# Kernel tuning notes

Hardware: AMD Instinct MI355X
Metric: run time of the kernel (lower is better)

The kernel has to match this reference:

```python
import jax, jax.numpy as jnp
import numpy as np

B, L, D = 2048, 64, 128
NODES = 512
EPS = 1e-6


def setup_inputs() -> dict:
    key = jax.random.key(0)
    ks = jax.random.split(key, 9)
    src_ids = jax.random.randint(ks[0], (B, L), 0, NODES, dtype=jnp.int32)
    dst_ids = jax.random.randint(ks[1], (B, L), 0, NODES, dtype=jnp.int32)
    src_node_ids = jax.random.randint(ks[2], (B,), 1, NODES, dtype=jnp.int32)
    dst_node_ids = jax.random.randint(ks[3], (B,), 1, NODES, dtype=jnp.int32)
    node_interact_times = 100.0 + jax.random.uniform(ks[4], (B,), jnp.float32)
    src_times = jax.random.uniform(ks[5], (B, L), jnp.float32) * 100.0
    dst_times = jax.random.uniform(ks[6], (B, L), jnp.float32) * 100.0
    W1 = jax.random.normal(ks[7], (1, D), jnp.float32) * 0.5
    b1 = jnp.zeros((D,), jnp.float32)
    W2 = jax.random.normal(ks[8], (D, D), jnp.float32) * (1.0 / np.sqrt(D))
    b2 = jnp.zeros((D,), jnp.float32)
    return dict(src_padded_nodes_neighbor_ids=src_ids,
                dst_padded_nodes_neighbor_ids=dst_ids,
                src_node_ids=src_node_ids, dst_node_ids=dst_node_ids,
                node_interact_times=node_interact_times,
                src_padded_nodes_neighbor_times=src_times,
                dst_padded_nodes_neighbor_times=dst_times,
                W1=W1, b1=b1, W2=W2, b2=b2)


def _group_stats(ids, t):
    # per-position stats of the group sharing the same neighbor id. ids,t: (L,)
    n_pos = ids.shape[0]
    eq = ids[:, None] == ids[None, :]                       # (L,L) group membership
    n = eq.sum(1)                                           # group size at each position
    nf = n.astype(t.dtype)
    tb = jnp.broadcast_to(t[None, :], (n_pos, n_pos))
    tmax = jnp.max(jnp.where(eq, tb, -jnp.inf), axis=1)
    tmin = jnp.min(jnp.where(eq, tb, jnp.inf), axis=1)
    # mean(diff(sorted(ts))) == (max-min)/(n-1)
    avg_iat = jnp.where(n > 1, (tmax - tmin) / jnp.maximum(nf - 1.0, 1.0), 0.0)
    # stable rank of each element inside its own group (order statistic)
    pos = jnp.arange(n_pos)
    before = (t[:, None] < t[None, :]) | ((t[:, None] == t[None, :]) & (pos[:, None] < pos[None, :]))
    rank = jnp.sum(eq & before, axis=0)
    split = n // 2
    sel = eq & (rank[None, :] == split[:, None])            # exactly one per group
    t_split = jnp.sum(jnp.where(sel, tb, 0.0), axis=1)      # sorted(ts)[n//2]
    denom = jnp.maximum(nf - split.astype(t.dtype) - 1.0, 1.0)
    recent_iat = jnp.where(n >= 4, (tmax - t_split) / denom, 0.0)
    valid = ids != 0                                        # dicts skip neighbor id 0
    return nf, jnp.where(valid, avg_iat, 0.0), jnp.where(valid, recent_iat, 0.0)


def _cross_lookup(ids_a, ids_b, vals_b):
    # dict.get(nid, 0.0) over the other side's per-group values (id 0 excluded)
    match = (ids_a[:, None] == ids_b[None, :]) & (ids_b[None, :] != 0)
    idx = jnp.argmax(match, axis=1)
    return jnp.where(match.any(1), vals_b[idx], 0.0)


def _last_time(ids_a, ids_b, t_b):
    # dict comprehension keeps the LAST occurrence's timestamp (id 0 excluded)
    match = (ids_a[:, None] == ids_b[None, :]) & (ids_b[None, :] != 0)
    score = jnp.where(match, jnp.arange(ids_b.shape[0])[None, :], -1)
    li = score.max(1)
    return jnp.where(li >= 0, t_b[jnp.maximum(li, 0)], 0.0)


def _side_features(ids_a, t_a, ids_b, t_b, other_node_id, cur_t,
                   n_a, avg_a, rec_a, avg_b, rec_b, other_first):
    ft = t_a.dtype
    c_self = n_a
    c_other = jnp.sum(ids_a[:, None] == ids_b[None, :], axis=1).astype(ft)
    is_other = (ids_a == other_node_id).astype(ft)
    connects = (c_other > 0).astype(ft)
    freq_asym = jnp.where(c_other > 0, c_self / (c_other + EPS), 0.0)
    rcy_self = cur_t - t_a
    rcy_other = cur_t - _last_time(ids_a, ids_b, t_b)
    temp_asym = jnp.where(rcy_self > EPS, rcy_other / (rcy_self + EPS), 0.0)
    iat_other = _cross_lookup(ids_a, ids_b, avg_b)
    iat_asym = jnp.where(iat_other > EPS, avg_a / (iat_other + EPS), 0.0)
    riat_other = _cross_lookup(ids_a, ids_b, rec_b)
    riat_asym = jnp.where(riat_other > EPS, rec_a / (riat_other + EPS), 0.0)
    if other_first:
        head = [c_other, c_self]
    else:
        head = [c_self, c_other]
    return jnp.stack(head + [is_other, connects, freq_asym, temp_asym, iat_asym, riat_asym], axis=1)


def _per_sample(ids_s, ids_d, sid, did, cur_t, t_s, t_d):
    n_s, avg_s, rec_s = _group_stats(ids_s, t_s)
    n_d, avg_d, rec_d = _group_stats(ids_d, t_d)
    f_src = _side_features(ids_s, t_s, ids_d, t_d, did, cur_t,
                           n_s, avg_s, rec_s, avg_d, rec_d, False)
    f_dst = _side_features(ids_d, t_d, ids_s, t_s, sid, cur_t,
                           n_d, avg_d, rec_d, avg_s, rec_s, True)
    return f_src, f_dst


def _mlp_sum(feats, W1, b1, W2, b2):
    # Linear(1->D) -> ReLU -> Linear(D->D), applied per scalar feature, summed over the 8 features
    h = jax.nn.relu(feats[..., None] * W1[0] + b1)           # [B,L,8,D]
    y = jnp.einsum('blfd,de->blfe', h, W2) + b2
    return y.sum(axis=2)                                      # [B,L,D]


def reference(src_padded_nodes_neighbor_ids, dst_padded_nodes_neighbor_ids,
              src_node_ids, dst_node_ids, node_interact_times,
              src_padded_nodes_neighbor_times, dst_padded_nodes_neighbor_times,
              W1, b1, W2, b2):
    f_src, f_dst = jax.vmap(_per_sample)(
        src_padded_nodes_neighbor_ids, dst_padded_nodes_neighbor_ids,
        src_node_ids, dst_node_ids, node_interact_times,
        src_padded_nodes_neighbor_times, dst_padded_nodes_neighbor_times)
    f_src = jnp.where((src_padded_nodes_neighbor_ids == 0)[..., None], 0.0, f_src)
    f_dst = jnp.where((dst_padded_nodes_neighbor_ids == 0)[..., None], 0.0, f_dst)
    src_path_features = _mlp_sum(f_src, W1, b1, W2, b2)
    dst_path_features = _mlp_sum(f_dst, W1, b1, W2, b2)
    return src_path_features, dst_path_features
```

## Files before the change

kernel.cpp:

```cpp
#include <hip/hip_runtime.h>


#define EPSF 1e-6f
#define LDB 136

typedef __attribute__((ext_vector_type(8))) short bf16x8;
typedef __attribute__((ext_vector_type(4))) float f32x4;
typedef __attribute__((ext_vector_type(2))) float f32x2;

__device__ inline short f2bf(float x) {
    unsigned u = __float_as_uint(x);
    return (short)((u + 0x7fffu + ((u >> 16) & 1u)) >> 16);
}

__global__ void w2t_prep(const float* __restrict__ W2, short* __restrict__ w2t) {
    const int idx = blockIdx.x * 256 + threadIdx.x;
    const int k = idx >> 7, n = idx & 127;
    w2t[n * 128 + k] = f2bf(W2[idx]);
}

__launch_bounds__(128)
__global__ void lpe_feats(const int* __restrict__ src_ids,
                          const int* __restrict__ dst_ids,
                          const int* __restrict__ src_nid,
                          const int* __restrict__ dst_nid,
                          const float* __restrict__ t_now,
                          const float* __restrict__ src_t,
                          const float* __restrict__ dst_t,
                          float* __restrict__ fs)
{
    __shared__ int2  s_idt[128];
    __shared__ __align__(16) f32x4 s_tab[2][512];

    const int tid  = threadIdx.x;
    const int b    = blockIdx.x;
    const int side = tid >> 6;
    const int i    = tid & 63;

    #pragma unroll
    for (int u = tid; u < 1024; u += 128) ((float*)s_tab)[u * 4] = 0.f;

    const float cur = t_now[b];
    const int   s_n = src_nid[b], d_n = dst_nid[b];

    const int*   idp = side ? dst_ids : src_ids;
    const float* tp  = side ? dst_t   : src_t;
    const int   my_id = idp[b * 64 + i];
    const float my_t  = tp [b * 64 + i];
    s_idt[tid] = make_int2(my_id, __float_as_int(my_t));
    __syncthreads();

    int n = 0, rank = 0, later = 0;
    float tmax = -3.4e38f, tmin = 3.4e38f;
    const int sbase = side * 64;
    #pragma unroll 8
    for (int j = 0; j < 64; ++j) {
        const int2 e = s_idt[sbase + j];
        const float tj = __int_as_float(e.y);
        if (e.x == my_id) {
            ++n;
            tmax = fmaxf(tmax, tj);
            tmin = fminf(tmin, tj);
            if (tj < my_t || (tj == my_t && j < i)) ++rank;
            if (j > i) later = 1;
        }
    }
    const float nf    = (float)n;
    const int   split = n >> 1;
    const float avg   = (n > 1) ? (tmax - tmin) / (nf - 1.f) : 0.f;
    if (my_id != 0) {
        s_tab[side][my_id].x = nf;
        s_tab[side][my_id].y = avg;
        if (rank == split)
            s_tab[side][my_id].z = (n >= 4)
                ? (tmax - my_t) / fmaxf(nf - (float)split - 1.f, 1.f) : 0.f;
        if (!later)
            s_tab[side][my_id].w = my_t;
    }
    __syncthreads();

    const int os = side ^ 1;
    const float rec_m = (my_id != 0) ? s_tab[side][my_id].z : 0.f;
    const f32x4 to = s_tab[os][my_id];
    const float n_o = (my_id != 0) ? to.x : 0.f;
    const bool  hit = n_o > 0.f;
    const float avg_o = hit ? to.y : 0.f;
    const float rec_o = hit ? to.z : 0.f;
    const float lastt = hit ? to.w : 0.f;
    const int other_node = side ? s_n : d_n;
    const float m = (my_id != 0) ? 1.f : 0.f;

    const float rcy_s = cur - my_t;
    const float rcy_o = cur - lastt;
    f32x4 f0, f1;
    f0.x = m * nf;
    f0.y = m * n_o;
    f0.z = m * ((my_id == other_node) ? 1.f : 0.f);
    f0.w = m * (hit ? 1.f : 0.f);
    f1.x = m * (hit ? nf / (n_o + EPSF) : 0.f);
    f1.y = m * ((rcy_s > EPSF) ? rcy_o / (rcy_s + EPSF) : 0.f);
    f1.z = m * ((avg_o > EPSF) ? avg / (avg_o + EPSF) : 0.f);
    f1.w = m * ((rec_o > EPSF) ? rec_m / (rec_o + EPSF) : 0.f);

    const long rowf = (long)side * 131072 + (long)b * 64 + i;
    *(f32x4*)&fs[rowf * 8]     = f0;
    *(f32x4*)&fs[rowf * 8 + 4] = f1;
}

__launch_bounds__(256, 3)
__global__ void lpe_gemm(const float* __restrict__ fs,
                         const short* __restrict__ w2t,
                         const float* __restrict__ W1,
                         const float* __restrict__ b1,
                         const float* __restrict__ b2,
                         float* __restrict__ out)
{
    __shared__ __align__(16) float s_w1[128], s_b1[128], s_b2[128];
    __shared__ __align__(16) short W2T[128 * LDB];
    __shared__ __align__(16) float s_stage[4][32][32];

    const int tid  = threadIdx.x;
    const int lane = tid & 63, wv = tid >> 6;
    const int quad = lane >> 4, ln = lane & 15;

    #pragma unroll
    for (int it = 0; it < 8; ++it) {
        const int c = tid + it * 256;
        const int n = c >> 4, j = c & 15;
        *(bf16x8*)&W2T[n * LDB + j * 8] = *(const bf16x8*)&w2t[n * 128 + j * 8];
    }
    if (tid < 128) { s_w1[tid] = W1[tid]; s_b1[tid] = b1[tid]; s_b2[tid] = b2[tid]; }
    __syncthreads();

    const long base = (long)blockIdx.x * 128;

    float fxr[2][8];
    #pragma unroll
    for (int rg = 0; rg < 2; ++rg) {
        const long rowf = base + wv * 32 + rg * 16 + ln;
        const f32x4 a = *(const f32x4*)&fs[rowf * 8];
        const f32x4 c = *(const f32x4*)&fs[rowf * 8 + 4];
        fxr[rg][0] = a.x; fxr[rg][1] = a.y; fxr[rg][2] = a.z; fxr[rg][3] = a.w;
        fxr[rg][4] = c.x; fxr[rg][5] = c.y; fxr[rg][6] = c.z; fxr[rg][7] = c.w;
    }

    bf16x8 gf[2][4];
    #pragma unroll
    for (int kk = 0; kk < 4; ++kk) {
        const int kb = kk * 32 + quad * 8;
        #pragma unroll
        for (int rg = 0; rg < 2; ++rg) {
            #pragma unroll
            for (int u2 = 0; u2 < 4; ++u2) {
                const f32x2 w  = *(const f32x2*)&s_w1[kb + u2 * 2];
                const f32x2 bb = *(const f32x2*)&s_b1[kb + u2 * 2];
                f32x2 sv = {0.f, 0.f};
                #pragma unroll
                for (int f = 0; f < 8; ++f) {
                    const f32x2 h = w * fxr[rg][f] + bb;
                    sv += __builtin_elementwise_max(h, (f32x2){0.f, 0.f});
                }
                gf[rg][kk][u2 * 2]     = f2bf(sv.x);
                gf[rg][kk][u2 * 2 + 1] = f2bf(sv.y);
            }
        }
    }

    float* st = &s_stage[wv][0][0];
    const int sw = ln & 7;

    #pragma unroll
    for (int p = 0; p < 4; ++p) {
        const int et0 = 2 * p, et1 = 2 * p + 1;
        bf16x8 afA[4], afB[4];
        #pragma unroll
        for (int kk = 0; kk < 4; ++kk) {
            afA[kk] = *(const bf16x8*)&W2T[(et0 * 16 + ln) * LDB + kk * 32 + quad * 8];
            afB[kk] = *(const bf16x8*)&W2T[(et1 * 16 + ln) * LDB + kk * 32 + quad * 8];
        }
        f32x4 accA[2] = {(f32x4){0.f,0.f,0.f,0.f}, (f32x4){0.f,0.f,0.f,0.f}};
        f32x4 accB[2] = {(f32x4){0.f,0.f,0.f,0.f}, (f32x4){0.f,0.f,0.f,0.f}};
        #pragma unroll
        for (int kk = 0; kk < 4; ++kk)
            #pragma unroll
            for (int rg = 0; rg < 2; ++rg) {
                accA[rg] = __builtin_amdgcn_mfma_f32_16x16x32_bf16(afA[kk], gf[rg][kk], accA[rg], 0, 0, 0);
                accB[rg] = __builtin_amdgcn_mfma_f32_16x16x32_bf16(afB[kk], gf[rg][kk], accB[rg], 0, 0, 0);
            }
        const f32x4 bA = *(const f32x4*)&s_b2[et0 * 16 + quad * 4] * 8.f;
        const f32x4 bB = *(const f32x4*)&s_b2[et1 * 16 + quad * 4] * 8.f;

        if (p)
            asm volatile("s_waitcnt lgkmcnt(0)" ::: "memory");
        #pragma unroll
        for (int rg = 0; rg < 2; ++rg) {
            const int row = rg * 16 + ln;
            *(f32x4*)&st[row * 32 + ((quad ^ sw) * 4)]       = accA[rg] + bA;
            *(f32x4*)&st[row * 32 + (((4 + quad) ^ sw) * 4)] = accB[rg] + bB;
        }
        asm volatile("s_waitcnt lgkmcnt(0)" ::: "memory");
        #pragma unroll
        for (int rr = 0; rr < 4; ++rr) {
            const int rl = rr * 8 + (lane >> 3);
            const f32x4 v = *(const f32x4*)&st[rl * 32 + (((lane & 7) ^ (rl & 7)) * 4)];
            const long rowf = base + wv * 32 + rl;
            __builtin_nontemporal_store(v,
                (f32x4*)&out[rowf * 128 + p * 32 + (lane & 7) * 4]);
        }
    }
}

__launch_bounds__(256, 2)
__global__ void lpe_fused4(const int* __restrict__ src_ids,
                           const int* __restrict__ dst_ids,
                           const int* __restrict__ src_nid,
                           const int* __restrict__ dst_nid,
                           const float* __restrict__ t_now,
                           const float* __restrict__ src_t,
                           const float* __restrict__ dst_t,
                           const float* __restrict__ W1,
                           const float* __restrict__ b1,
                           const float* __restrict__ W2,
                           const float* __restrict__ b2,
                           float* __restrict__ out)
{
    __shared__ int2  s_idt[128];
    __shared__ __align__(16) f32x4 s_tab[2][512];
    __shared__ float s_feats[128][9];
    __shared__ __align__(16) float s_w1[128], s_b1[128], s_b2[128];
    __shared__ __align__(16) float s_stage[4][32][32];
    __shared__ __align__(16) short W2T[128 * LDB];

    const int tid  = threadIdx.x;
    const int b4   = blockIdx.x * 4;
    const int lane = tid & 63, wv = tid >> 6;
    const int quad = lane >> 4, ln = lane & 15;
    const int side = (tid >> 6) & 1;
    const int i    = tid & 63;

    if (tid < 128) { s_w1[tid] = W1[tid]; s_b1[tid] = b1[tid]; s_b2[tid] = b2[tid]; }
    for (int u = tid; u < 16384; u += 256) {
        const int k = u >> 7, n = u & 127;
        W2T[n * LDB + k] = f2bf(W2[u]);
    }
    const int*   idp = side ? dst_ids : src_ids;
    const float* tp  = side ? dst_t   : src_t;
    int   pf_id = 0; float pf_t = 0.f;
    if (tid < 128) { pf_id = idp[b4 * 64 + i]; pf_t = tp[b4 * 64 + i]; }
    float cur = t_now[b4];
    int   s_n = src_nid[b4], d_n = dst_nid[b4];
    for (int u = tid; u < 1024; u += 256) ((float*)s_tab)[u * 4] = 0.f;
    const long side_stride = 2048L * 64L * 128L;

    for (int s = 0; s < 4; ++s) {
        const int   my_id = pf_id;  const float my_t = pf_t;
        const float curs  = cur;    const int sns = s_n, dns = d_n;
        if (tid < 128) s_idt[tid] = make_int2(my_id, __float_as_int(my_t));
        __syncthreads();

        float nf = 0.f, avg = 0.f;
        if (tid < 128) {
            int n = 0, rank = 0, later = 0;
            float tmax = -3.4e38f, tmin = 3.4e38f;
            const int sbase = side * 64;
            #pragma unroll 8
            for (int j = 0; j < 64; ++j) {
                const int2 e = s_idt[sbase + j];
                const float tj = __int_as_float(e.y);
                if (e.x == my_id) {
                    ++n; tmax = fmaxf(tmax, tj); tmin = fminf(tmin, tj);
                    if (tj < my_t || (tj == my_t && j < i)) ++rank;
                    if (j > i) later = 1;
                }
            }
            nf = (float)n;
            const int split = n >> 1;
            avg = (n > 1) ? (tmax - tmin) / (nf - 1.f) : 0.f;
            if (my_id != 0) {
                s_tab[side][my_id].x = nf;
                s_tab[side][my_id].y = avg;
                if (rank == split)
                    s_tab[side][my_id].z = (n >= 4)
                        ? (tmax - my_t) / fmaxf(nf - (float)split - 1.f, 1.f) : 0.f;
                if (!later) s_tab[side][my_id].w = my_t;
            }
        }
        if (s < 3) {
            if (tid < 128) {
                pf_id = idp[(b4 + s + 1) * 64 + i];
                pf_t  = tp [(b4 + s + 1) * 64 + i];
            }
            cur = t_now[b4 + s + 1];
            s_n = src_nid[b4 + s + 1];
            d_n = dst_nid[b4 + s + 1];
        }
        __syncthreads();

        if (tid < 128) {
            const int os = side ^ 1;
            const float rec_m = (my_id != 0) ? s_tab[side][my_id].z : 0.f;
            const f32x4 to = s_tab[os][my_id];
            const float n_o = (my_id != 0) ? to.x : 0.f;
            const bool  hit = n_o > 0.f;
            const float avg_o = hit ? to.y : 0.f;
            const float rec_o = hit ? to.z : 0.f;
            const float lastt = hit ? to.w : 0.f;
            const int other_node = side ? sns : dns;
            const float m = (my_id != 0) ? 1.f : 0.f;
            const float rcy_s = curs - my_t;
            const float rcy_o = curs - lastt;
            s_feats[tid][0] = m * nf;
            s_feats[tid][1] = m * n_o;
            s_feats[tid][2] = m * ((my_id == other_node) ? 1.f : 0.f);
            s_feats[tid][3] = m * (hit ? 1.f : 0.f);
            s_feats[tid][4] = m * (hit ? nf / (n_o + EPSF) : 0.f);
            s_feats[tid][5] = m * ((rcy_s > EPSF) ? rcy_o / (rcy_s + EPSF) : 0.f);
            s_feats[tid][6] = m * ((avg_o > EPSF) ? avg / (avg_o + EPSF) : 0.f);
            s_feats[tid][7] = m * ((rec_o > EPSF) ? rec_m / (rec_o + EPSF) : 0.f);
        }
        __syncthreads();

        float fxr[2][8];
        #pragma unroll
        for (int rg = 0; rg < 2; ++rg) {
            const int row = wv * 32 + rg * 16 + ln;
            #pragma unroll
            for (int j = 0; j < 8; ++j) fxr[rg][j] = s_feats[row][j];
        }
        if (s < 3)
            for (int u = tid; u < 1024; u += 256) ((float*)s_tab)[u * 4] = 0.f;

        bf16x8 gf[2][4];
        #pragma unroll
        for (int kk = 0; kk < 4; ++kk) {
            const int kb = kk * 32 + quad * 8;
            #pragma unroll
            for (int rg = 0; rg < 2; ++rg) {
                #pragma unroll
                for (int u2 = 0; u2 < 4; ++u2) {
                    const f32x2 w  = *(const f32x2*)&s_w1[kb + u2 * 2];
                    const f32x2 bb = *(const f32x2*)&s_b1[kb + u2 * 2];
                    f32x2 sv = {0.f, 0.f};
                    #pragma unroll
                    for (int f = 0; f < 8; ++f) {
                        const f32x2 h = w * fxr[rg][f] + bb;
                        sv += __builtin_elementwise_max(h, (f32x2){0.f, 0.f});
                    }
                    gf[rg][kk][u2 * 2]     = f2bf(sv.x);
                    gf[rg][kk][u2 * 2 + 1] = f2bf(sv.y);
                }
            }
        }

        float* st = &s_stage[wv][0][0];
        const int sw = ln & 7;
        const long rowbase = (long)(b4 + s) * 64;

        #pragma unroll
        for (int p = 0; p < 4; ++p) {
            const int et0 = 2 * p, et1 = 2 * p + 1;
            bf16x8 afA[4], afB[4];
            #pragma unroll
            for (int kk = 0; kk < 4; ++kk) {
                afA[kk] = *(const bf16x8*)&W2T[(et0 * 16 + ln) * LDB + kk * 32 + quad * 8];
                afB[kk] = *(const bf16x8*)&W2T[(et1 * 16 + ln) * LDB + kk * 32 + quad * 8];
            }
            f32x4 accA[2] = {(f32x4){0.f,0.f,0.f,0.f}, (f32x4){0.f,0.f,0.f,0.f}};
            f32x4 accB[2] = {(f32x4){0.f,0.f,0.f,0.f}, (f32x4){0.f,0.f,0.f,0.f}};
            #pragma unroll
            for (int kk = 0; kk < 4; ++kk)
                #pragma unroll
                for (int rg = 0; rg < 2; ++rg) {
                    accA[rg] = __builtin_amdgcn_mfma_f32_16x16x32_bf16(afA[kk], gf[rg][kk], accA[rg], 0, 0, 0);
                    accB[rg] = __builtin_amdgcn_mfma_f32_16x16x32_bf16(afB[kk], gf[rg][kk], accB[rg], 0, 0, 0);
                }
            const f32x4 bA = *(const f32x4*)&s_b2[et0 * 16 + quad * 4] * 8.f;
            const f32x4 bB = *(const f32x4*)&s_b2[et1 * 16 + quad * 4] * 8.f;

            if (p)
                asm volatile("s_waitcnt lgkmcnt(0)" ::: "memory");
            #pragma unroll
            for (int rg = 0; rg < 2; ++rg) {
                const int row = rg * 16 + ln;
                *(f32x4*)&st[row * 32 + ((quad ^ sw) * 4)]       = accA[rg] + bA;
                *(f32x4*)&st[row * 32 + (((4 + quad) ^ sw) * 4)] = accB[rg] + bB;
            }
            asm volatile("s_waitcnt lgkmcnt(0)" ::: "memory");
            #pragma unroll
            for (int rr = 0; rr < 4; ++rr) {
                const int rl = rr * 8 + (lane >> 3);
                const f32x4 v = *(const f32x4*)&st[rl * 32 + (((lane & 7) ^ (rl & 7)) * 4)];
                const int row = wv * 32 + rl;
                const int sd = row >> 6, ii = row & 63;
                __builtin_nontemporal_store(v,
                    (f32x4*)&out[(long)sd * side_stride + (rowbase + ii) * 128
                                 + p * 32 + (lane & 7) * 4]);
            }
        }
    }
}

extern "C" void kernel_launch(void* const* d_in, const int* in_sizes, int n_in,
                              void* d_out, int out_size, void* d_ws, size_t ws_size,
                              hipStream_t stream) {
    (void)in_sizes; (void)n_in; (void)out_size;
    const int*   src_ids = (const int*)  d_in[0];
    const int*   dst_ids = (const int*)  d_in[1];
    const int*   src_nid = (const int*)  d_in[2];
    const int*   dst_nid = (const int*)  d_in[3];
    const float* t_now   = (const float*)d_in[4];
    const float* src_t   = (const float*)d_in[5];
    const float* dst_t   = (const float*)d_in[6];
    const float* W1      = (const float*)d_in[7];
    const float* b1      = (const float*)d_in[8];
    const float* W2      = (const float*)d_in[9];
    const float* b2      = (const float*)d_in[10];
    float* out = (float*)d_out;

    const size_t W2T_BYTES  = 128 * 128 * sizeof(short);
    const size_t FEAT_BYTES = 262144ULL * 8 * sizeof(float);

    if (ws_size >= W2T_BYTES + FEAT_BYTES) {
        short* w2t = (short*)d_ws;
        float* fs  = (float*)((char*)d_ws + W2T_BYTES);
        w2t_prep<<<64, 256, 0, stream>>>(W2, w2t);
        lpe_feats<<<2048, 128, 0, stream>>>(src_ids, dst_ids, src_nid, dst_nid,
                                            t_now, src_t, dst_t, fs);
        lpe_gemm<<<2048, 256, 0, stream>>>(fs, w2t, W1, b1, b2, out);
    } else {
        lpe_fused4<<<512, 256, 0, stream>>>(src_ids, dst_ids, src_nid, dst_nid,
                                            t_now, src_t, dst_t, W1, b1, W2, b2, out);
    }
}
```

Measured before the change: 185.3 us.

## Fold W2 transpose into GEMM kernel, process two tiles per block, drop LDS staging

Removes the separate w2t_prep launch, so each GEMM block now reads fp32 W2 directly, converts it to bf16 and writes it transposed into LDS. The grid is halved and each block handles two 128-row chunks, which spreads the W2 load cost over more work, and the first chunk's feature loads are issued before the W2 load. The LDS staging buffer for output is removed: MFMA results are stored straight to global memory in 16-byte pieces instead of coalesced 128-byte rows. Occupancy hint rises to 4 blocks per CU. In exchange, every block performs strided fp32 W2 reads and the output stores are less coalesced.

```diff
diff --git a/kernel.cpp b/kernel.cpp
--- a/kernel.cpp
+++ b/kernel.cpp
@@ -11,12 +11,6 @@
 __device__ inline short f2bf(float x) {
     unsigned u = __float_as_uint(x);
     return (short)((u + 0x7fffu + ((u >> 16) & 1u)) >> 16);
-}
-
-__global__ void w2t_prep(const float* __restrict__ W2, short* __restrict__ w2t) {
-    const int idx = blockIdx.x * 256 + threadIdx.x;
-    const int k = idx >> 7, n = idx & 127;
-    w2t[n * 128 + k] = f2bf(W2[idx]);
 }
 
 __launch_bounds__(128)
@@ -107,9 +101,9 @@
     *(f32x4*)&fs[rowf * 8 + 4] = f1;
 }
 
-__launch_bounds__(256, 3)
+__launch_bounds__(256, 4)
 __global__ void lpe_gemm(const float* __restrict__ fs,
-                         const short* __restrict__ w2t,
+                         const float* __restrict__ W2,
                          const float* __restrict__ W1,
                          const float* __restrict__ b1,
                          const float* __restrict__ b2,
@@ -117,95 +111,97 @@
 {
     __shared__ __align__(16) float s_w1[128], s_b1[128], s_b2[128];
     __shared__ __align__(16) short W2T[128 * LDB];
-    __shared__ __align__(16) float s_stage[4][32][32];
 
     const int tid  = threadIdx.x;
     const int lane = tid & 63, wv = tid >> 6;
     const int quad = lane >> 4, ln = lane & 15;
 
+    f32x4 fa0[2], fb0[2];
     #pragma unroll
-    for (int it = 0; it < 8; ++it) {
-        const int c = tid + it * 256;
-        const int n = c >> 4, j = c & 15;
-        *(bf16x8*)&W2T[n * LDB + j * 8] = *(const bf16x8*)&w2t[n * 128 + j * 8];
+    for (int rg = 0; rg < 2; ++rg) {
+        const long rowf = (long)blockIdx.x * 128 + wv * 32 + rg * 16 + ln;
+        fa0[rg] = *(const f32x4*)&fs[rowf * 8];
+        fb0[rg] = *(const f32x4*)&fs[rowf * 8 + 4];
+    }
+
+    for (int v = tid; v < 8192; v += 256) {
+        const int kp = v >> 7, n = v & 127;
+        const float a = W2[(2 * kp)     * 128 + n];
+        const float c = W2[(2 * kp + 1) * 128 + n];
+        const unsigned pk = (unsigned)(unsigned short)f2bf(a)
+                          | ((unsigned)(unsigned short)f2bf(c) << 16);
+        *(unsigned*)&W2T[n * LDB + 2 * kp] = pk;
     }
     if (tid < 128) { s_w1[tid] = W1[tid]; s_b1[tid] = b1[tid]; s_b2[tid] = b2[tid]; }
     __syncthreads();
 
-    const long base = (long)blockIdx.x * 128;
-
-    float fxr[2][8];
-    #pragma unroll
-    for (int rg = 0; rg < 2; ++rg) {
-        const long rowf = base + wv * 32 + rg * 16 + ln;
-        const f32x4 a = *(const f32x4*)&fs[rowf * 8];
-        const f32x4 c = *(const f32x4*)&fs[rowf * 8 + 4];
-        fxr[rg][0] = a.x; fxr[rg][1] = a.y; fxr[rg][2] = a.z; fxr[rg][3] = a.w;
-        fxr[rg][4] = c.x; fxr[rg][5] = c.y; fxr[rg][6] = c.z; fxr[rg][7] = c.w;
-    }
-
-    bf16x8 gf[2][4];
-    #pragma unroll
-    for (int kk = 0; kk < 4; ++kk) {
-        const int kb = kk * 32 + quad * 8;
-        #pragma unroll
-        for (int rg = 0; rg < 2; ++rg) {
-            #pragma unroll
-            for (int u2 = 0; u2 < 4; ++u2) {
-                const f32x2 w  = *(const f32x2*)&s_w1[kb + u2 * 2];
-                const f32x2 bb = *(const f32x2*)&s_b1[kb + u2 * 2];
-                f32x2 sv = {0.f, 0.f};
-                #pragma unroll
-                for (int f = 0; f < 8; ++f) {
-                    const f32x2 h = w * fxr[rg][f] + bb;
-                    sv += __builtin_elementwise_max(h, (f32x2){0.f, 0.f});
-                }
-                gf[rg][kk][u2 * 2]     = f2bf(sv.x);
-                gf[rg][kk][u2 * 2 + 1] = f2bf(sv.y);
-            }
-        }
-    }
-
-    float* st = &s_stage[wv][0][0];
-    const int sw = ln & 7;
-
-    #pragma unroll
-    for (int p = 0; p < 4; ++p) {
-        const int et0 = 2 * p, et1 = 2 * p + 1;
-        bf16x8 afA[4], afB[4];
+    #pragma unroll 2
+    for (int ch = 0; ch < 2; ++ch) {
+        const long base = (long)(blockIdx.x + ch * 1024) * 128;
+
+        float fxr[2][8];
+        if (ch == 0) {
+            #pragma unroll
+            for (int rg = 0; rg < 2; ++rg) {
+                fxr[rg][0] = fa0[rg].x; fxr[rg][1] = fa0[rg].y;
+                fxr[rg][2] = fa0[rg].z; fxr[rg][3] = fa0[rg].w;
+                fxr[rg][4] = fb0[rg].x; fxr[rg][5] = fb0[rg].y;
+                fxr[rg][6] = fb0[rg].z; fxr[rg][7] = fb0[rg].w;
+            }
+        } else {
+            #pragma unroll
+            for (int rg = 0; rg < 2; ++rg) {
+                const long rowf = base + wv * 32 + rg * 16 + ln;
+                const f32x4 a = *(const f32x4*)&fs[rowf * 8];
+                const f32x4 c = *(const f32x4*)&fs[rowf * 8 + 4];
+                fxr[rg][0] = a.x; fxr[rg][1] = a.y; fxr[rg][2] = a.z; fxr[rg][3] = a.w;
+                fxr[rg][4] = c.x; fxr[rg][5] = c.y; fxr[rg][6] = c.z; fxr[rg][7] = c.w;
+            }
+        }
+
+        bf16x8 gf[2][4];
         #pragma unroll
         for (int kk = 0; kk < 4; ++kk) {
-            afA[kk] = *(const bf16x8*)&W2T[(et0 * 16 + ln) * LDB + kk * 32 + quad * 8];
-            afB[kk] = *(const bf16x8*)&W2T[(et1 * 16 + ln) * LDB + kk * 32 + quad * 8];
-        }
-        f32x4 accA[2] = {(f32x4){0.f,0.f,0.f,0.f}, (f32x4){0.f,0.f,0.f,0.f}};
-        f32x4 accB[2] = {(f32x4){0.f,0.f,0.f,0.f}, (f32x4){0.f,0.f,0.f,0.f}};
+            const int kb = kk * 32 + quad * 8;
+            #pragma unroll
+            for (int rg = 0; rg < 2; ++rg) {
+                #pragma unroll
+                for (int u2 = 0; u2 < 4; ++u2) {
+                    const f32x2 w  = *(const f32x2*)&s_w1[kb + u2 * 2];
+                    const f32x2 bb = *(const f32x2*)&s_b1[kb + u2 * 2];
+                    f32x2 sv = {0.f, 0.f};
+                    #pragma unroll
+                    for (int f = 0; f < 8; ++f) {
+                        const f32x2 h = w * fxr[rg][f] + bb;
+                        sv += __builtin_elementwise_max(h, (f32x2){0.f, 0.f});
+                    }
+                    gf[rg][kk][u2 * 2]     = f2bf(sv.x);
+                    gf[rg][kk][u2 * 2 + 1] = f2bf(sv.y);
+                }
+            }
+        }
+
         #pragma unroll
-        for (int kk = 0; kk < 4; ++kk)
-            #pragma unroll
-            for (int rg = 0; rg < 2; ++rg) {
-                accA[rg] = __builtin_amdgcn_mfma_f32_16x16x32_bf16(afA[kk], gf[rg][kk], accA[rg], 0, 0, 0);
-                accB[rg] = __builtin_amdgcn_mfma_f32_16x16x32_bf16(afB[kk], gf[rg][kk], accB[rg], 0, 0, 0);
-            }
-        const f32x4 bA = *(const f32x4*)&s_b2[et0 * 16 + quad * 4] * 8.f;
-        const f32x4 bB = *(const f32x4*)&s_b2[et1 * 16 + quad * 4] * 8.f;
-
-        if (p)
-            asm volatile("s_waitcnt lgkmcnt(0)" ::: "memory");
-        #pragma unroll
-        for (int rg = 0; rg < 2; ++rg) {
-            const int row = rg * 16 + ln;
-            *(f32x4*)&st[row * 32 + ((quad ^ sw) * 4)]       = accA[rg] + bA;
-            *(f32x4*)&st[row * 32 + (((4 + quad) ^ sw) * 4)] = accB[rg] + bB;
-        }
-        asm volatile("s_waitcnt lgkmcnt(0)" ::: "memory");
-        #pragma unroll
-        for (int rr = 0; rr < 4; ++rr) {
-            const int rl = rr * 8 + (lane >> 3);
-            const f32x4 v = *(const f32x4*)&st[rl * 32 + (((lane & 7) ^ (rl & 7)) * 4)];
-            const long rowf = base + wv * 32 + rl;
-            __builtin_nontemporal_store(v,
-                (f32x4*)&out[rowf * 128 + p * 32 + (lane & 7) * 4]);
+        for (int et = 0; et < 8; ++et) {
+            bf16x8 af[4];
+            #pragma unroll
+            for (int kk = 0; kk < 4; ++kk)
+                af[kk] = *(const bf16x8*)&W2T[(et * 16 + ln) * LDB + kk * 32 + quad * 8];
+            f32x4 acc[2] = {(f32x4){0.f,0.f,0.f,0.f}, (f32x4){0.f,0.f,0.f,0.f}};
+            #pragma unroll
+            for (int kk = 0; kk < 4; ++kk)
+                #pragma unroll
+                for (int rg = 0; rg < 2; ++rg)
+                    acc[rg] = __builtin_amdgcn_mfma_f32_16x16x32_bf16(af[kk], gf[rg][kk], acc[rg], 0, 0, 0);
+
+            const int e0 = et * 16 + quad * 4;
+            const f32x4 badd = *(const f32x4*)&s_b2[e0] * 8.f;
+            #pragma unroll
+            for (int rg = 0; rg < 2; ++rg) {
+                const long rowf = base + wv * 32 + rg * 16 + ln;
+                __builtin_nontemporal_store(acc[rg] + badd,
+                    (f32x4*)&out[rowf * 128 + e0]);
+            }
         }
     }
 }
@@ -417,16 +413,13 @@
     const float* b2      = (const float*)d_in[10];
     float* out = (float*)d_out;
 
-    const size_t W2T_BYTES  = 128 * 128 * sizeof(short);
     const size_t FEAT_BYTES = 262144ULL * 8 * sizeof(float);
 
-    if (ws_size >= W2T_BYTES + FEAT_BYTES) {
-        short* w2t = (short*)d_ws;
-        float* fs  = (float*)((char*)d_ws + W2T_BYTES);
-        w2t_prep<<<64, 256, 0, stream>>>(W2, w2t);
+    if (ws_size >= FEAT_BYTES) {
+        float* fs = (float*)d_ws;
         lpe_feats<<<2048, 128, 0, stream>>>(src_ids, dst_ids, src_nid, dst_nid,
                                             t_now, src_t, dst_t, fs);
-        lpe_gemm<<<2048, 256, 0, stream>>>(fs, w2t, W1, b1, b2, out);
+        lpe_gemm<<<1024, 256, 0, stream>>>(fs, W2, W1, b1, b2, out);
     } else {
         lpe_fused4<<<512, 256, 0, stream>>>(src_ids, dst_ids, src_nid, dst_nid,
                                             t_now, src_t, dst_t, W1, b1, W2, b2, out);
```

After: 214.5 us. 1.16x slower.
